# Optimization experiments

Hardware: AMD Instinct MI355X
Metric: run time of the kernel (lower is better)

## Reference

```python
import jax, jax.numpy as jnp
import numpy as np

B, S, DIM, HEADS = 4, 2048, 1024, 16
SCALE = float((DIM // HEADS) ** 0.5)  # sqrt(d_k) = 8.0
EPS = 1e-5


def _ln(h, g, b):
    m = jnp.mean(h, axis=-1, keepdims=True)
    v = jnp.mean((h - m) ** 2, axis=-1, keepdims=True)
    return (h - m) * jax.lax.rsqrt(v + EPS) * g + b


def setup_inputs() -> dict:
    key = jax.random.key(0)
    ks = jax.random.split(key, 16)
    w = lambda k: jax.random.normal(k, (DIM, DIM), jnp.float32) * 0.02
    vec = lambda k: jax.random.normal(k, (DIM,), jnp.float32) * 0.02
    return {
        "x": jax.random.normal(ks[0], (B, S, DIM), jnp.float32),
        "Wq": w(ks[1]), "bq": vec(ks[2]),
        "Wk": w(ks[3]), "bk": vec(ks[4]),
        "Wv": w(ks[5]), "bv": vec(ks[6]),
        "g_at": 1.0 + vec(ks[7]), "b_at": vec(ks[8]),
        "g_ln": 1.0 + vec(ks[9]), "b_ln": vec(ks[10]),
        "W1": w(ks[11]), "c1": vec(ks[12]),
        "W2": w(ks[13]), "c2": vec(ks[14]),
    }


def reference(x, Wq, bq, Wk, bk, Wv, bv, g_at, b_at, g_ln, b_ln, W1, c1, W2, c2):
    # --- MultiHeadAttention (single-head math: no head reshape in source) ---
    Q = x @ Wq + bq                                   # [B,S,D]
    K = x @ Wk + bk
    V = x @ Wv + bv
    scores = jax.nn.softmax(jnp.einsum('bqd,bkd->bqk', Q, K) / SCALE, axis=-1)
    at = _ln(jnp.einsum('bqk,bkd->bqd', scores, V) + x, g_at, b_at)
    # --- EncoderStack ---
    h = _ln(at + x, g_ln, b_ln)
    res = h
    # note: source's `if i != len(self.ffn)` is always True -> GELU on every layer
    h = jax.nn.gelu(h @ W1 + c1, approximate=False)
    h = jax.nn.gelu(h @ W2 + c2, approximate=False)
    return _ln(h + res, g_ln, b_ln)
```

## Files before the change

### kernel.cpp

```cpp
#include <hip/hip_runtime.h>
#include <cstdint>
#include <cstddef>

#define DIMN 1024
#define SEQ  2048
#define NBAT 4
#define TOKS (NBAT * SEQ)

typedef unsigned short u16;
typedef unsigned int   u32;

typedef __bf16 bf16x8 __attribute__((ext_vector_type(8)));
typedef float  f32x4  __attribute__((ext_vector_type(4)));

#define AS1 __attribute__((address_space(1)))
#define AS3 __attribute__((address_space(3)))


__device__ __forceinline__ u16 f2b(float f) {
  union { float f; u32 u; } v; v.f = f;
  u32 r = v.u + 0x7fffu + ((v.u >> 16) & 1u);
  return (u16)(r >> 16);
}

__device__ __forceinline__ float b2f(u16 b) {
  union { u32 u; float f; } v; v.u = ((u32)b) << 16;
  return v.f;
}

__device__ __forceinline__ float gelu_exact(float v) {
  return 0.5f * v * (1.0f + erff(v * 0.70710678118654752f));
}

__device__ __forceinline__ void blk_sum2(float& a, float& b, float* sm) {
  #pragma unroll
  for (int o = 32; o >= 1; o >>= 1) {
    a += __shfl_xor(a, o, 64);
    b += __shfl_xor(b, o, 64);
  }
  int w = threadIdx.x >> 6;
  if ((threadIdx.x & 63) == 0) { sm[w] = a; sm[4 + w] = b; }
  __syncthreads();
  a = sm[0] + sm[1] + sm[2] + sm[3];
  b = sm[4] + sm[5] + sm[6] + sm[7];
  __syncthreads();
}

__device__ __forceinline__ float blk_max(float a, float* sm) {
  #pragma unroll
  for (int o = 32; o >= 1; o >>= 1) a = fmaxf(a, __shfl_xor(a, o, 64));
  int w = threadIdx.x >> 6;
  if ((threadIdx.x & 63) == 0) sm[w] = a;
  __syncthreads();
  float r = fmaxf(fmaxf(sm[0], sm[1]), fmaxf(sm[2], sm[3]));
  __syncthreads();
  return r;
}

__device__ __forceinline__ float blk_sum1(float a, float* sm) {
  #pragma unroll
  for (int o = 32; o >= 1; o >>= 1) a += __shfl_xor(a, o, 64);
  int w = threadIdx.x >> 6;
  if ((threadIdx.x & 63) == 0) sm[w] = a;
  __syncthreads();
  float r = sm[0] + sm[1] + sm[2] + sm[3];
  __syncthreads();
  return r;
}


__global__ __launch_bounds__(256) void conv_x(const float* __restrict__ x,
                                              u16* __restrict__ xb) {
  size_t i = ((size_t)blockIdx.x * 256 + threadIdx.x) * 4;
  float4 v = *(const float4*)(x + i);
  uint2 o;
  o.x = (u32)f2b(v.x) | ((u32)f2b(v.y) << 16);
  o.y = (u32)f2b(v.z) | ((u32)f2b(v.w) << 16);
  *(uint2*)(xb + i) = o;
}

__global__ __launch_bounds__(256) void transpose_w5(
    const float* __restrict__ Wq, const float* __restrict__ Wk,
    const float* __restrict__ Wv, const float* __restrict__ W1,
    const float* __restrict__ W2,
    u16* __restrict__ Wqkv, u16* __restrict__ W1T, u16* __restrict__ W2T)
{
  const float* W; u16* T;
  switch (blockIdx.z) {
    case 0: W = Wq; T = Wqkv;                      break;
    case 1: W = Wk; T = Wqkv + 1 * DIMN * DIMN;    break;
    case 2: W = Wv; T = Wqkv + 2 * DIMN * DIMN;    break;
    case 3: W = W1; T = W1T;                       break;
    default: W = W2; T = W2T;                      break;
  }
  __shared__ float t[32][33];
  int tx = threadIdx.x, ty = threadIdx.y;
  int k0 = blockIdx.x * 32, n0 = blockIdx.y * 32;
  #pragma unroll
  for (int j = 0; j < 32; j += 8)
    t[ty + j][tx] = W[(size_t)(k0 + ty + j) * DIMN + n0 + tx];
  __syncthreads();
  #pragma unroll
  for (int j = 0; j < 32; j += 8)
    T[(size_t)(n0 + ty + j) * DIMN + k0 + tx] = f2b(t[tx][ty + j]);
}

__global__ __launch_bounds__(256) void transpose_v(const u16* __restrict__ Vb,
                                                   u16* __restrict__ VT) {
  __shared__ u16 t[32][33];
  int tx = threadIdx.x, ty = threadIdx.y;
  int d0 = blockIdx.x * 32, t0 = blockIdx.y * 32;
  const u16* src = Vb + (size_t)blockIdx.z * SEQ * DIMN;
  u16*       dst = VT + (size_t)blockIdx.z * DIMN * SEQ;
  #pragma unroll
  for (int j = 0; j < 32; j += 8)
    t[ty + j][tx] = src[(size_t)(t0 + ty + j) * DIMN + d0 + tx];
  __syncthreads();
  #pragma unroll
  for (int j = 0; j < 32; j += 8)
    dst[(size_t)(d0 + ty + j) * SEQ + t0 + tx] = t[tx][ty + j];
}

template <int EPI, int SWZ>
__global__ __launch_bounds__(256) void gemm_bt(
    const u16* __restrict__ A, const u16* __restrict__ Bm,
    u16* __restrict__ Cb, u16* __restrict__ Cb2, u16* __restrict__ Cb3,
    const float* __restrict__ bias, const float* __restrict__ bias2,
    const float* __restrict__ bias3,
    int M, int N, int K, int ldc,
    size_t sA, size_t sB, size_t sC)
{
  __shared__ u16 As[128 * 64];
  __shared__ u16 Bs[128 * 64];

  const int tid = threadIdx.x;

  int bm0, bn0;
  if (SWZ == 1) {
    const int id   = blockIdx.y * gridDim.x + blockIdx.x;
    const int xcd  = id & 7;
    const int idx  = id >> 3;
    const int band = gridDim.x >> 3;
    const int bm_l = idx % band;
    const int bn   = idx / band;
    bm0 = (xcd * band + bm_l) * 128;
    bn0 = bn * 128;
  } else {
    bm0 = blockIdx.x * 128;
    bn0 = blockIdx.y * 128;
  }

  A  += (size_t)blockIdx.z * sA;
  Bm += (size_t)blockIdx.z * sB;
  const int wave = tid >> 6, lane = tid & 63;
  const int wm   = (wave >> 1) * 64, wn = (wave & 1) * 64;
  const int l16  = lane & 15, quad = lane >> 4;

  f32x4 acc[4][4] = {};

  for (int k0 = 0; k0 < K; k0 += 64) {
    #pragma unroll
    for (int j = 0; j < 4; ++j) {
      const int c  = wave * 256 + j * 64 + lane;
      const int r  = c >> 3;
      const int cg = (c & 7) ^ (r & 7);
      const u16* gA = A  + (size_t)(bm0 + r) * K + k0 + cg * 8;
      const u16* gB = Bm + (size_t)(bn0 + r) * K + k0 + cg * 8;
      u16* lA = As + (wave * 4 + j) * 512;
      u16* lB = Bs + (wave * 4 + j) * 512;
      __builtin_amdgcn_global_load_lds((const AS1 void*)gA, (AS3 void*)lA, 16, 0, 0);
      __builtin_amdgcn_global_load_lds((const AS1 void*)gB, (AS3 void*)lB, 16, 0, 0);
    }
    __syncthreads();

    #pragma unroll
    for (int kk = 0; kk < 64; kk += 32) {
      const int kc = kk >> 3;
      const int sw = l16 & 7;
      bf16x8 af[4], bfr[4];
      #pragma unroll
      for (int t = 0; t < 4; ++t) {
        const int row = wm + t * 16 + l16;
        af[t] = *(const bf16x8*)(&As[row * 64 + (((kc + quad) ^ sw) << 3)]);
      }
      #pragma unroll
      for (int t = 0; t < 4; ++t) {
        const int row = wn + t * 16 + l16;
        bfr[t] = *(const bf16x8*)(&Bs[row * 64 + (((kc + quad) ^ sw) << 3)]);
      }
      #pragma unroll
      for (int mt = 0; mt < 4; ++mt)
        #pragma unroll
        for (int nt = 0; nt < 4; ++nt)
          acc[mt][nt] = __builtin_amdgcn_mfma_f32_16x16x32_bf16(
              af[mt], bfr[nt], acc[mt][nt], 0, 0, 0);
    }
    __syncthreads();
  }

  u16* Cbz = Cb + (size_t)blockIdx.z * sC;

  #pragma unroll
  for (int mt = 0; mt < 4; ++mt) {
    int grow0 = bm0 + wm + mt * 16 + quad * 4;
    #pragma unroll
    for (int nt = 0; nt < 4; ++nt) {
      int gcol = bn0 + wn + nt * 16 + l16;
      if (EPI == 3) {
        const int seg = gcol >> 10;
        const int col = gcol & 1023;
        const float* bp = (seg == 0) ? bias : (seg == 1) ? bias2 : bias3;
        u16*         cp = (seg == 0) ? Cb   : (seg == 1) ? Cb2   : Cb3;
        float bv = bp[col];
        #pragma unroll
        for (int r = 0; r < 4; ++r)
          cp[(size_t)(grow0 + r) * ldc + col] = f2b(acc[mt][nt][r] + bv);
      } else if (EPI == 4) {
        float bv = bias[gcol];
        #pragma unroll
        for (int r = 0; r < 4; ++r)
          Cbz[(size_t)(grow0 + r) * ldc + gcol] =
              f2b(gelu_exact(acc[mt][nt][r] + bv));
      } else {
        #pragma unroll
        for (int r = 0; r < 4; ++r)
          Cbz[(size_t)(grow0 + r) * ldc + gcol] = f2b(acc[mt][nt][r]);
      }
    }
  }
}

__global__ __launch_bounds__(256) void softmax_rows(const u16* __restrict__ Sc,
                                                    u16* __restrict__ P) {
  __shared__ float sm[8];
  int row = blockIdx.x, t = threadIdx.x;
  const u16* s = Sc + (size_t)row * SEQ;
  uint4 raw = *(const uint4*)(s + t * 8);
  float v[8];
  #pragma unroll
  for (int m = 0; m < 4; ++m) {
    u32 w = ((const u32*)&raw)[m];
    v[2 * m]     = b2f((u16)(w & 0xffff)) * 0.125f;
    v[2 * m + 1] = b2f((u16)(w >> 16)) * 0.125f;
  }
  float mx = -1e30f;
  #pragma unroll
  for (int i = 0; i < 8; ++i) mx = fmaxf(mx, v[i]);
  mx = blk_max(mx, sm);
  float sum = 0.0f;
  #pragma unroll
  for (int i = 0; i < 8; ++i) { v[i] = __expf(v[i] - mx); sum += v[i]; }
  sum = blk_sum1(sum, sm);
  float inv = 1.0f / sum;
  uint4 o;
  #pragma unroll
  for (int m = 0; m < 4; ++m)
    ((u32*)&o)[m] = (u32)f2b(v[2 * m] * inv) | ((u32)f2b(v[2 * m + 1] * inv) << 16);
  *(uint4*)(P + (size_t)row * SEQ + t * 8) = o;
}

__global__ __launch_bounds__(256) void ln1_fused(
    const u16* __restrict__ attn, const u16* __restrict__ xb,
    const float* __restrict__ g_at, const float* __restrict__ b_at,
    const float* __restrict__ g_ln, const float* __restrict__ b_ln,
    u16* __restrict__ hres)
{
  __shared__ float sm[8];
  int row = blockIdx.x, t = threadIdx.x;
  size_t base = (size_t)row * DIMN;
  uint2 ar = *(const uint2*)(attn + base + t * 4);
  uint2 xr4 = *(const uint2*)(xb + base + t * 4);
  float y[4], xr[4];
  float s = 0.0f, s2 = 0.0f;
  #pragma unroll
  for (int i = 0; i < 4; ++i) {
    u32 aw = ((const u32*)&ar)[i >> 1];
    u32 xw = ((const u32*)&xr4)[i >> 1];
    float av = b2f((u16)((i & 1) ? (aw >> 16) : (aw & 0xffff)));
    xr[i]    = b2f((u16)((i & 1) ? (xw >> 16) : (xw & 0xffff)));
    y[i] = av + xr[i];
    s += y[i]; s2 += y[i] * y[i];
  }
  blk_sum2(s, s2, sm);
  float m  = s * (1.0f / DIMN);
  float rs = rsqrtf(s2 * (1.0f / DIMN) - m * m + 1e-5f);
  float z[4];
  s = 0.0f; s2 = 0.0f;
  #pragma unroll
  for (int i = 0; i < 4; ++i) {
    int c = t * 4 + i;
    float at = (y[i] - m) * rs * g_at[c] + b_at[c];
    z[i] = at + xr[i];
    s += z[i]; s2 += z[i] * z[i];
  }
  blk_sum2(s, s2, sm);
  float m2  = s * (1.0f / DIMN);
  float rs2 = rsqrtf(s2 * (1.0f / DIMN) - m2 * m2 + 1e-5f);
  uint2 o;
  #pragma unroll
  for (int i = 0; i < 2; ++i) {
    int c = t * 4 + 2 * i;
    float h0 = (z[2 * i]     - m2) * rs2 * g_ln[c]     + b_ln[c];
    float h1 = (z[2 * i + 1] - m2) * rs2 * g_ln[c + 1] + b_ln[c + 1];
    ((u32*)&o)[i] = (u32)f2b(h0) | ((u32)f2b(h1) << 16);
  }
  *(uint2*)(hres + base + t * 4) = o;
}

__global__ __launch_bounds__(256) void ln2_final(
    const u16* __restrict__ u, const u16* __restrict__ hres,
    const float* __restrict__ g, const float* __restrict__ bb,
    float* __restrict__ out)
{
  __shared__ float sm[8];
  int row = blockIdx.x, t = threadIdx.x;
  size_t base = (size_t)row * DIMN;
  uint2 ur = *(const uint2*)(u + base + t * 4);
  uint2 hr = *(const uint2*)(hres + base + t * 4);
  float y[4];
  float s = 0.0f, s2 = 0.0f;
  #pragma unroll
  for (int i = 0; i < 4; ++i) {
    u32 uw = ((const u32*)&ur)[i >> 1];
    u32 hw = ((const u32*)&hr)[i >> 1];
    float uv = b2f((u16)((i & 1) ? (uw >> 16) : (uw & 0xffff)));
    float hv = b2f((u16)((i & 1) ? (hw >> 16) : (hw & 0xffff)));
    y[i] = uv + hv;
    s += y[i]; s2 += y[i] * y[i];
  }
  blk_sum2(s, s2, sm);
  float m  = s * (1.0f / DIMN);
  float rs = rsqrtf(s2 * (1.0f / DIMN) - m * m + 1e-5f);
  float4 o;
  o.x = (y[0] - m) * rs * g[t * 4 + 0] + bb[t * 4 + 0];
  o.y = (y[1] - m) * rs * g[t * 4 + 1] + bb[t * 4 + 1];
  o.z = (y[2] - m) * rs * g[t * 4 + 2] + bb[t * 4 + 2];
  o.w = (y[3] - m) * rs * g[t * 4 + 3] + bb[t * 4 + 3];
  *(float4*)(out + base + t * 4) = o;
}


extern "C" void kernel_launch(void* const* d_in, const int* in_sizes, int n_in,
                              void* d_out, int out_size, void* d_ws, size_t ws_size,
                              hipStream_t stream)
{
  const float* x    = (const float*)d_in[0];
  const float* Wq   = (const float*)d_in[1];
  const float* bq   = (const float*)d_in[2];
  const float* Wk   = (const float*)d_in[3];
  const float* bk   = (const float*)d_in[4];
  const float* Wv   = (const float*)d_in[5];
  const float* bv   = (const float*)d_in[6];
  const float* g_at = (const float*)d_in[7];
  const float* b_at = (const float*)d_in[8];
  const float* g_ln = (const float*)d_in[9];
  const float* b_ln = (const float*)d_in[10];
  const float* W1   = (const float*)d_in[11];
  const float* c1   = (const float*)d_in[12];
  const float* W2   = (const float*)d_in[13];
  const float* c2   = (const float*)d_in[14];
  float* out = (float*)d_out;

  char* ws = (char*)d_ws;
  const size_t MB = 1u << 20;
  u16* xb    = (u16*)(ws + 0 * MB);
  u16* W1T   = (u16*)(ws + 16 * MB);
  u16* W2T   = (u16*)(ws + 18 * MB);
  u16* WqkvT = (u16*)(ws + 20 * MB);
  u16* Qb    = (u16*)(ws + 26 * MB);
  u16* Kb    = (u16*)(ws + 42 * MB);
  u16* Vb    = (u16*)(ws + 58 * MB);
  u16* VT    = (u16*)(ws + 74 * MB);
  u16* Sc    = (u16*)(ws + 90 * MB);
  u16* attn  = (u16*)(ws + 90 * MB);
  u16* hres  = (u16*)(ws + 106 * MB);
  u16* Pb    = (u16*)(ws + 122 * MB);
  u16* tb    = Kb;
  u16* ub    = Vb;

  conv_x<<<(TOKS * DIMN) / 1024, 256, 0, stream>>>(x, xb);
  transpose_w5<<<dim3(32, 32, 5), dim3(32, 8), 0, stream>>>(
      Wq, Wk, Wv, W1, W2, WqkvT, W1T, W2T);

  gemm_bt<3, 1><<<dim3(64, 24), 256, 0, stream>>>(
      xb, WqkvT, Qb, Kb, Vb, bq, bk, bv,
      TOKS, 3 * DIMN, DIMN, DIMN, 0, 0, 0);

  transpose_v<<<dim3(32, 64, NBAT), dim3(32, 8), 0, stream>>>(Vb, VT);

  gemm_bt<6, 0><<<dim3(16, 16, NBAT), 256, 0, stream>>>(
      Qb, Kb, Sc, nullptr, nullptr, nullptr, nullptr, nullptr,
      SEQ, SEQ, DIMN, SEQ,
      (size_t)SEQ * DIMN, (size_t)SEQ * DIMN, (size_t)SEQ * SEQ);
  softmax_rows<<<TOKS, 256, 0, stream>>>(Sc, Pb);
  gemm_bt<6, 0><<<dim3(16, 8, NBAT), 256, 0, stream>>>(
      Pb, VT, attn, nullptr, nullptr, nullptr, nullptr, nullptr,
      SEQ, DIMN, SEQ, DIMN,
      (size_t)SEQ * SEQ, (size_t)DIMN * SEQ, (size_t)SEQ * DIMN);

  ln1_fused<<<TOKS, 256, 0, stream>>>(attn, xb, g_at, b_at, g_ln, b_ln, hres);

  gemm_bt<4, 1><<<dim3(64, 8), 256, 0, stream>>>(
      hres, W1T, tb, nullptr, nullptr, c1, nullptr, nullptr,
      TOKS, DIMN, DIMN, DIMN, 0, 0, 0);
  gemm_bt<4, 1><<<dim3(64, 8), 256, 0, stream>>>(
      tb, W2T, ub, nullptr, nullptr, c2, nullptr, nullptr,
      TOKS, DIMN, DIMN, DIMN, 0, 0, 0);

  ln2_final<<<TOKS, 256, 0, stream>>>(ub, hres, g_ln, b_ln, out);
}
```

Before: 382.6 us.

## Fuse V transpose into QKV GEMM epilogue and merge prep kernels

The QKV GEMM blocks that produce V now stage their output tile in shared memory with an XOR swizzle and write it out transposed, straight into the VT layout. This removes the separate transpose_v kernel and its extra round trip of V through global memory. The x-to-bf16 conversion and the weight transposes are also merged into a single launch to save one kernel launch. The cost is extra shared-memory traffic and a barrier in the V-tile epilogue, plus a less uniform mix of block types in the prep kernel.

```diff
diff --git a/kernel.cpp b/kernel.cpp
--- a/kernel.cpp
+++ b/kernel.cpp
@@ -68,33 +68,38 @@
   return r;
 }
 
-
-__global__ __launch_bounds__(256) void conv_x(const float* __restrict__ x,
-                                              u16* __restrict__ xb) {
-  size_t i = ((size_t)blockIdx.x * 256 + threadIdx.x) * 4;
-  float4 v = *(const float4*)(x + i);
-  uint2 o;
-  o.x = (u32)f2b(v.x) | ((u32)f2b(v.y) << 16);
-  o.y = (u32)f2b(v.z) | ((u32)f2b(v.w) << 16);
-  *(uint2*)(xb + i) = o;
-}
-
-__global__ __launch_bounds__(256) void transpose_w5(
+__global__ __launch_bounds__(256) void prep_all(
+    const float* __restrict__ x,
     const float* __restrict__ Wq, const float* __restrict__ Wk,
     const float* __restrict__ Wv, const float* __restrict__ W1,
     const float* __restrict__ W2,
+    u16* __restrict__ xb,
     u16* __restrict__ Wqkv, u16* __restrict__ W1T, u16* __restrict__ W2T)
 {
+  __shared__ float t[32][33];
+  const int tx = threadIdx.x, ty = threadIdx.y;
+  if (blockIdx.z == 5) {
+    const int tid = ty * 32 + tx;
+    const size_t base = ((size_t)(blockIdx.y * 32 + blockIdx.x)) * 8192;
+    #pragma unroll
+    for (int it = 0; it < 8; ++it) {
+      size_t i = base + (size_t)(it * 256 + tid) * 4;
+      float4 v = *(const float4*)(x + i);
+      uint2 o;
+      o.x = (u32)f2b(v.x) | ((u32)f2b(v.y) << 16);
+      o.y = (u32)f2b(v.z) | ((u32)f2b(v.w) << 16);
+      *(uint2*)(xb + i) = o;
+    }
+    return;
+  }
   const float* W; u16* T;
   switch (blockIdx.z) {
-    case 0: W = Wq; T = Wqkv;                      break;
-    case 1: W = Wk; T = Wqkv + 1 * DIMN * DIMN;    break;
-    case 2: W = Wv; T = Wqkv + 2 * DIMN * DIMN;    break;
-    case 3: W = W1; T = W1T;                       break;
-    default: W = W2; T = W2T;                      break;
-  }
-  __shared__ float t[32][33];
-  int tx = threadIdx.x, ty = threadIdx.y;
+    case 0: W = Wq; T = Wqkv;                   break;
+    case 1: W = Wk; T = Wqkv + 1 * DIMN * DIMN; break;
+    case 2: W = Wv; T = Wqkv + 2 * DIMN * DIMN; break;
+    case 3: W = W1; T = W1T;                    break;
+    default: W = W2; T = W2T;                   break;
+  }
   int k0 = blockIdx.x * 32, n0 = blockIdx.y * 32;
   #pragma unroll
   for (int j = 0; j < 32; j += 8)
@@ -103,22 +108,6 @@
   #pragma unroll
   for (int j = 0; j < 32; j += 8)
     T[(size_t)(n0 + ty + j) * DIMN + k0 + tx] = f2b(t[tx][ty + j]);
-}
-
-__global__ __launch_bounds__(256) void transpose_v(const u16* __restrict__ Vb,
-                                                   u16* __restrict__ VT) {
-  __shared__ u16 t[32][33];
-  int tx = threadIdx.x, ty = threadIdx.y;
-  int d0 = blockIdx.x * 32, t0 = blockIdx.y * 32;
-  const u16* src = Vb + (size_t)blockIdx.z * SEQ * DIMN;
-  u16*       dst = VT + (size_t)blockIdx.z * DIMN * SEQ;
-  #pragma unroll
-  for (int j = 0; j < 32; j += 8)
-    t[ty + j][tx] = src[(size_t)(t0 + ty + j) * DIMN + d0 + tx];
-  __syncthreads();
-  #pragma unroll
-  for (int j = 0; j < 32; j += 8)
-    dst[(size_t)(d0 + ty + j) * SEQ + t0 + tx] = t[tx][ty + j];
 }
 
 template <int EPI, int SWZ>
@@ -130,8 +119,9 @@
     int M, int N, int K, int ldc,
     size_t sA, size_t sB, size_t sC)
 {
-  __shared__ u16 As[128 * 64];
-  __shared__ u16 Bs[128 * 64];
+  __shared__ u16 smem[2 * 128 * 64];
+  u16* As = smem;
+  u16* Bs = smem + 128 * 64;
 
   const int tid = threadIdx.x;
 
@@ -141,10 +131,8 @@
     const int xcd  = id & 7;
     const int idx  = id >> 3;
     const int band = gridDim.x >> 3;
-    const int bm_l = idx % band;
-    const int bn   = idx / band;
-    bm0 = (xcd * band + bm_l) * 128;
-    bn0 = bn * 128;
+    bm0 = (xcd * band + idx % band) * 128;
+    bn0 = (idx / band) * 128;
   } else {
     bm0 = blockIdx.x * 128;
     bn0 = blockIdx.y * 128;
@@ -198,8 +186,40 @@
     __syncthreads();
   }
 
+  if (EPI == 3 && (bn0 >> 10) == 2) {
+    #pragma unroll
+    for (int mt = 0; mt < 4; ++mt) {
+      const int tok_l0 = wm + mt * 16 + quad * 4;
+      #pragma unroll
+      for (int nt = 0; nt < 4; ++nt) {
+        const int d_l = wn + nt * 16 + l16;
+        const float bv = bias3[(bn0 & 1023) + d_l];
+        ushort4 pk;
+        pk.x = f2b(acc[mt][nt][0] + bv);
+        pk.y = f2b(acc[mt][nt][1] + bv);
+        pk.z = f2b(acc[mt][nt][2] + bv);
+        pk.w = f2b(acc[mt][nt][3] + bv);
+        const int addr = d_l * 128 +
+            ((((tok_l0 >> 3) ^ (d_l & 7)) << 3) | (tok_l0 & 7));
+        *(ushort4*)(&smem[addr]) = pk;
+      }
+    }
+    __syncthreads();
+    const int b_idx = bm0 >> 11;
+    const int tok0  = bm0 & 2047;
+    const int d0    = bn0 & 1023;
+    u16* dst = Cb3 + (size_t)b_idx * DIMN * SEQ;
+    #pragma unroll
+    for (int p = 0; p < 8; ++p) {
+      const int idx = p * 256 + tid;
+      const int row = idx >> 4, c = idx & 15;
+      uint4 v = *(const uint4*)(&smem[row * 128 + ((c ^ (row & 7)) << 3)]);
+      *(uint4*)(&dst[(size_t)(d0 + row) * SEQ + tok0 + c * 8]) = v;
+    }
+    return;
+  }
+
   u16* Cbz = Cb + (size_t)blockIdx.z * sC;
-
   #pragma unroll
   for (int mt = 0; mt < 4; ++mt) {
     int grow0 = bm0 + wm + mt * 16 + quad * 4;
@@ -209,8 +229,8 @@
       if (EPI == 3) {
         const int seg = gcol >> 10;
         const int col = gcol & 1023;
-        const float* bp = (seg == 0) ? bias : (seg == 1) ? bias2 : bias3;
-        u16*         cp = (seg == 0) ? Cb   : (seg == 1) ? Cb2   : Cb3;
+        const float* bp = (seg == 0) ? bias : bias2;
+        u16*         cp = (seg == 0) ? Cb   : Cb2;
         float bv = bp[col];
         #pragma unroll
         for (int r = 0; r < 4; ++r)
@@ -369,24 +389,20 @@
   u16* WqkvT = (u16*)(ws + 20 * MB);
   u16* Qb    = (u16*)(ws + 26 * MB);
   u16* Kb    = (u16*)(ws + 42 * MB);
-  u16* Vb    = (u16*)(ws + 58 * MB);
-  u16* VT    = (u16*)(ws + 74 * MB);
-  u16* Sc    = (u16*)(ws + 90 * MB);
-  u16* attn  = (u16*)(ws + 90 * MB);
-  u16* hres  = (u16*)(ws + 106 * MB);
-  u16* Pb    = (u16*)(ws + 122 * MB);
+  u16* VT    = (u16*)(ws + 58 * MB);
+  u16* Sc    = (u16*)(ws + 74 * MB);
+  u16* attn  = (u16*)(ws + 74 * MB);
+  u16* hres  = (u16*)(ws + 90 * MB);
+  u16* Pb    = (u16*)(ws + 106 * MB);
   u16* tb    = Kb;
-  u16* ub    = Vb;
-
-  conv_x<<<(TOKS * DIMN) / 1024, 256, 0, stream>>>(x, xb);
-  transpose_w5<<<dim3(32, 32, 5), dim3(32, 8), 0, stream>>>(
-      Wq, Wk, Wv, W1, W2, WqkvT, W1T, W2T);
+  u16* ub    = VT;
+
+  prep_all<<<dim3(32, 32, 6), dim3(32, 8), 0, stream>>>(
+      x, Wq, Wk, Wv, W1, W2, xb, WqkvT, W1T, W2T);
 
   gemm_bt<3, 1><<<dim3(64, 24), 256, 0, stream>>>(
-      xb, WqkvT, Qb, Kb, Vb, bq, bk, bv,
+      xb, WqkvT, Qb, Kb, VT, bq, bk, bv,
       TOKS, 3 * DIMN, DIMN, DIMN, 0, 0, 0);
-
-  transpose_v<<<dim3(32, 64, NBAT), dim3(32, 8), 0, stream>>>(Vb, VT);
 
   gemm_bt<6, 0><<<dim3(16, 16, NBAT), 256, 0, stream>>>(
       Qb, Kb, Sc, nullptr, nullptr, nullptr, nullptr, nullptr,
```

New measurement: 386.6 us. About the same (+1.1%).
